# Optimization experiments

Measured on AMD Instinct MI355X. Metric: run time of the kernel, lower is better.

Reference implementation:

```python
import jax, jax.numpy as jnp
import numpy as np

B, H, W, C = 32, 56, 56, 384
NH, WS, SS = 12, 7, 3
DH = C // NH
N = WS * WS
HID = 4 * C
SCALE = DH ** -0.5


def _make_attn_mask(h, w, ws, ss):
    img = np.zeros((h, w), dtype=np.float32)
    cnt = 0
    for hs in (slice(0, -ws), slice(-ws, -ss), slice(-ss, None)):
        for wsl in (slice(0, -ws), slice(-ws, -ss), slice(-ss, None)):
            img[hs, wsl] = cnt
            cnt += 1
    mw = img.reshape(h // ws, ws, w // ws, ws).transpose(0, 2, 1, 3).reshape(-1, ws * ws)
    diff = mw[:, None, :] - mw[:, :, None]  # (nW, n, n)
    return np.where(diff != 0, np.float32(-100.0), np.float32(0.0))


def _make_rel_pos_index(ws):
    coords = np.stack(np.meshgrid(np.arange(ws), np.arange(ws), indexing='ij')).reshape(2, -1)
    rel = (coords[:, :, None] - coords[:, None, :]).transpose(1, 2, 0)  # (n, n, 2)
    rel[..., 0] += ws - 1
    rel[..., 1] += ws - 1
    rel[..., 0] *= 2 * ws - 1
    return rel.sum(-1)  # (n, n)


ATTN_MASK = jnp.asarray(_make_attn_mask(H, W, WS, SS))          # (nW, n, n)
REL_IDX = jnp.asarray(_make_rel_pos_index(WS))                   # (n, n)


def layernorm(x, g, b, eps):
    mu = jnp.mean(x, axis=-1, keepdims=True)
    var = jnp.var(x, axis=-1, keepdims=True)
    return (x - mu) * jax.lax.rsqrt(var + eps) * g + b


def window_partition(x, ws):
    b, h, w, c = x.shape
    x = x.reshape(b, h // ws, ws, w // ws, ws, c)
    return x.transpose(0, 1, 3, 2, 4, 5).reshape(-1, ws, ws, c)


def window_reverse(windows, ws, h, w):
    b = windows.shape[0] // ((h // ws) * (w // ws))
    x = windows.reshape(b, h // ws, w // ws, ws, ws, -1)
    return x.transpose(0, 1, 3, 2, 4, 5).reshape(b, h, w, -1)


def setup_inputs() -> dict:
    key = jax.random.key(0)
    ks = jax.random.split(key, 8)
    d = {
        'x': jax.random.normal(ks[0], (B, H * W, C), dtype=jnp.float32),
        'ln1_g': jnp.ones((C,), jnp.float32), 'ln1_b': jnp.zeros((C,), jnp.float32),
        'qkv_w': jax.random.normal(ks[1], (C, 3 * C), jnp.float32) * 0.02,
        'qkv_b': jnp.zeros((3 * C,), jnp.float32),
        'proj_w': jax.random.normal(ks[2], (C, C), jnp.float32) * 0.02,
        'proj_b': jnp.zeros((C,), jnp.float32),
        'rpb_table': jax.random.normal(ks[3], ((2 * WS - 1) ** 2, NH), jnp.float32) * 0.02,
        'ln2_g': jnp.ones((C,), jnp.float32), 'ln2_b': jnp.zeros((C,), jnp.float32),
        'ffln_g': jnp.ones((C,), jnp.float32), 'ffln_b': jnp.zeros((C,), jnp.float32),
        'ff1_w': jax.random.normal(ks[4], (C, HID), jnp.float32) * 0.02,
        'ff1_b': jnp.zeros((HID,), jnp.float32),
        'ff2_w': jax.random.normal(ks[5], (HID, C), jnp.float32) * 0.02,
        'ff2_b': jnp.zeros((C,), jnp.float32),
    }
    return d


def reference(x, ln1_g, ln1_b, qkv_w, qkv_b, proj_w, proj_b, rpb_table,
              ln2_g, ln2_b, ffln_g, ffln_b, ff1_w, ff1_b, ff2_w, ff2_b):
    b = x.shape[0]
    shortcut = x
    xn = layernorm(x, ln1_g, ln1_b, 1e-5).reshape(b, H, W, C)
    shifted = jnp.roll(xn, shift=(-SS, -SS), axis=(1, 2))
    xw = window_partition(shifted, WS).reshape(-1, N, C)  # (b*nW, n, c)
    Bw = xw.shape[0]
    nW = Bw // b

    qkv = (xw @ qkv_w + qkv_b).reshape(Bw, N, 3, NH, DH).transpose(2, 0, 3, 1, 4)
    q, k, v = qkv[0], qkv[1], qkv[2]  # (Bw, nh, n, dh)
    dots = jnp.einsum('bhnd,bhmd->bhnm', q, k) * SCALE

    bias = rpb_table[REL_IDX.reshape(-1)].reshape(N, N, NH).transpose(2, 0, 1)  # (nh, n, n)
    attn = dots + bias[None]
    attn = attn.reshape(b, nW, NH, N, N) + ATTN_MASK[None, :, None, :, :]
    attn = jax.nn.softmax(attn.reshape(Bw, NH, N, N), axis=-1)

    out = jnp.einsum('bhnm,bhmd->bhnd', attn, v)
    out = out.transpose(0, 2, 1, 3).reshape(Bw, N, C)
    out = out @ proj_w + proj_b

    out = window_reverse(out.reshape(-1, WS, WS, C), WS, H, W)
    out = jnp.roll(out, shift=(SS, SS), axis=(1, 2)).reshape(b, H * W, C)

    x = shortcut + out
    y = layernorm(x, ln2_g, ln2_b, 1e-5)
    y = layernorm(y, ffln_g, ffln_b, 1e-6)
    y = jax.nn.gelu(y @ ff1_w + ff1_b, approximate=False) @ ff2_w + ff2_b
    return x + y
```

## Files before the change

kernel.cpp:

```cpp
#include <hip/hip_runtime.h>
#include <hip/hip_bf16.h>

typedef short bf16x8 __attribute__((ext_vector_type(8)));
typedef short short4v __attribute__((ext_vector_type(4)));
typedef float f32x4  __attribute__((ext_vector_type(4)));

static constexpr float SCALE = 0.17677669529663687f;

__device__ __forceinline__ void gload_lds16(const void* g, void* l) {
  __builtin_amdgcn_global_load_lds(
      (const __attribute__((address_space(1))) unsigned int*)g,
      (__attribute__((address_space(3))) unsigned int*)l, 16, 0, 0);
}

__device__ __forceinline__ size_t win_to_nat(int t) {
  int win = t / 49; int n = t - win * 49;
  int bb = win >> 6; int wimg = win & 63;
  int hb = wimg >> 3, wb = wimg & 7;
  int nr = n / 7, nc = n - nr * 7;
  int hh = hb * 7 + nr + 3; if (hh >= 56) hh -= 56;
  int ww = wb * 7 + nc + 3; if (ww >= 56) ww -= 56;
  return (size_t)bb * 3136 + (size_t)hh * 56 + ww;
}

__device__ __forceinline__ float gelu_tanh(float val) {
  float u = val * (val * val * 0.044715f + 1.0f) * 1.5957691216f;
  float e = __expf(u);
  float th = 1.f - 2.f / (e + 1.f);
  return 0.5f * val * (1.f + th);
}

__global__ __launch_bounds__(256)
void k_transpose(const float* __restrict__ W, __hip_bfloat16* __restrict__ Wt,
                 int K, int N) {
  __shared__ float tile[32][33];
  int tx = threadIdx.x & 31, ty = threadIdx.x >> 5;
  int tc = blockIdx.x, tr = blockIdx.y;
#pragma unroll
  for (int r = 0; r < 32; r += 8)
    tile[r + ty][tx] = W[(size_t)(tr * 32 + r + ty) * N + tc * 32 + tx];
  __syncthreads();
#pragma unroll
  for (int r = 0; r < 32; r += 8)
    Wt[(size_t)(tc * 32 + r + ty) * K + tr * 32 + tx] =
        __float2bfloat16(tile[tx][r + ty]);
}

__global__ __launch_bounds__(256)
void k_ln1(const float* __restrict__ x, const float* __restrict__ gw,
           const float* __restrict__ bw, __hip_bfloat16* __restrict__ xw) {
  int lane = threadIdx.x & 63;
  int t = blockIdx.x * 4 + (threadIdx.x >> 6);
  size_t nt = win_to_nat(t);
  const float* xr = x + nt * 384;
  float4 a  = *(const float4*)(xr + lane * 4);
  float2 c2 = *(const float2*)(xr + 256 + lane * 2);
  float v[6] = {a.x, a.y, a.z, a.w, c2.x, c2.y};
  int c0 = lane * 4, c1 = 256 + lane * 2;
  int ch[6] = {c0, c0 + 1, c0 + 2, c0 + 3, c1, c1 + 1};
  float s = 0.f, q = 0.f;
#pragma unroll
  for (int i = 0; i < 6; i++) { s += v[i]; q += v[i] * v[i]; }
#pragma unroll
  for (int m = 1; m < 64; m <<= 1) { s += __shfl_xor(s, m); q += __shfl_xor(q, m); }
  float mean = s * (1.f / 384.f);
  float rstd = rsqrtf(q * (1.f / 384.f) - mean * mean + 1e-5f);
  __hip_bfloat16* o = xw + (size_t)t * 384;
#pragma unroll
  for (int i = 0; i < 6; i++)
    o[ch[i]] = __float2bfloat16((v[i] - mean) * rstd * gw[ch[i]] + bw[ch[i]]);
}

__global__ __launch_bounds__(256)
void k_ln2ff(const float* __restrict__ xres, const float* __restrict__ g2,
             const float* __restrict__ b2, const float* __restrict__ gf,
             const float* __restrict__ bf_, __hip_bfloat16* __restrict__ yln) {
  int lane = threadIdx.x & 63;
  int t = blockIdx.x * 4 + (threadIdx.x >> 6);
  const float* xr = xres + (size_t)t * 384;
  float4 a  = *(const float4*)(xr + lane * 4);
  float2 c2 = *(const float2*)(xr + 256 + lane * 2);
  float v[6] = {a.x, a.y, a.z, a.w, c2.x, c2.y};
  int c0 = lane * 4, c1 = 256 + lane * 2;
  int ch[6] = {c0, c0 + 1, c0 + 2, c0 + 3, c1, c1 + 1};
  float s = 0.f, q = 0.f;
#pragma unroll
  for (int i = 0; i < 6; i++) { s += v[i]; q += v[i] * v[i]; }
#pragma unroll
  for (int m = 1; m < 64; m <<= 1) { s += __shfl_xor(s, m); q += __shfl_xor(q, m); }
  float mean = s * (1.f / 384.f);
  float rstd = rsqrtf(q * (1.f / 384.f) - mean * mean + 1e-5f);
  float y1[6];
  s = 0.f; q = 0.f;
#pragma unroll
  for (int i = 0; i < 6; i++) {
    y1[i] = (v[i] - mean) * rstd * g2[ch[i]] + b2[ch[i]];
    s += y1[i]; q += y1[i] * y1[i];
  }
#pragma unroll
  for (int m = 1; m < 64; m <<= 1) { s += __shfl_xor(s, m); q += __shfl_xor(q, m); }
  float m2 = s * (1.f / 384.f);
  float r2 = rsqrtf(q * (1.f / 384.f) - m2 * m2 + 1e-6f);
  __hip_bfloat16* o = yln + (size_t)t * 384;
#pragma unroll
  for (int i = 0; i < 6; i++)
    o[ch[i]] = __float2bfloat16((y1[i] - m2) * r2 * gf[ch[i]] + bf_[ch[i]]);
}

enum { EPI_QKV = 0, EPI_PROJ = 1, EPI_FF1 = 2, EPI_FF2 = 3 };

template <int EPI>
__global__ __launch_bounds__(256)
void k_gemm(const __hip_bfloat16* __restrict__ A, const __hip_bfloat16* __restrict__ Wt,
            const float* __restrict__ bias, int K, int nCol, int cpx,
            const float* __restrict__ aux,
            float* __restrict__ out_f,
            __hip_bfloat16* __restrict__ out_b) {
  __shared__ __hip_bfloat16 LB[32768];
  int tid = threadIdx.x;
  int lane = tid & 63, w = tid >> 6;
  int g = lane >> 4, r16 = lane & 15;
  int wr = w >> 1, wc = w & 1;

  int bid = blockIdx.x;
  int wg = (bid & 7) * cpx + (bid >> 3);
  int rB = wg / nCol;
  int rowBlk = rB * 128;
  int colBlk = (wg - rB * nCol) * 128;

  int srow = tid >> 3;
  int cch = (tid & 7) ^ (srow & 7);
  const __hip_bfloat16* PA = A + (size_t)(rowBlk + srow) * K + cch * 8;
  const __hip_bfloat16* PB = Wt + (size_t)(colBlk + srow) * K + cch * 8;

#define STG(NB, T)                                                            \
  {                                                                           \
    int k0s = (T) << 6;                                                       \
    _Pragma("unroll") for (int j = 0; j < 4; j++) {                           \
      gload_lds16(PA + (size_t)j * 32 * K + k0s, &LB[(NB) * 8192 + j * 2048 + w * 512]); \
      gload_lds16(PB + (size_t)j * 32 * K + k0s, &LB[16384 + (NB) * 8192 + j * 2048 + w * 512]); \
    }                                                                         \
  }

  int aBase = (wr * 64 + r16) * 64;
  int bBase = (wc * 64 + r16) * 64;
  int sw0 = (g ^ (r16 & 7)) * 8;
  int sw1 = ((4 + g) ^ (r16 & 7)) * 8;

  f32x4 acc[4][4] = {};
  const int nt = K >> 6;

  STG(0, 0)

  for (int t = 0; t < nt; ++t) {
    int cur = t & 1;
    if (t + 1 < nt) {
      STG(cur ^ 1, t + 1)
      asm volatile("s_waitcnt vmcnt(8)" ::: "memory");
    } else {
      asm volatile("s_waitcnt vmcnt(0)" ::: "memory");
    }
    __builtin_amdgcn_s_barrier();

    bf16x8 a0[4], a1[4], b0[4], b1[4];
#pragma unroll
    for (int mi = 0; mi < 4; mi++) {
      a0[mi] = *(const bf16x8*)(&LB[cur * 8192 + aBase + mi * 1024 + sw0]);
      a1[mi] = *(const bf16x8*)(&LB[cur * 8192 + aBase + mi * 1024 + sw1]);
    }
#pragma unroll
    for (int ni = 0; ni < 4; ni++) {
      b0[ni] = *(const bf16x8*)(&LB[16384 + cur * 8192 + bBase + ni * 1024 + sw0]);
      b1[ni] = *(const bf16x8*)(&LB[16384 + cur * 8192 + bBase + ni * 1024 + sw1]);
    }
    __builtin_amdgcn_s_setprio(1);
#pragma unroll
    for (int mi = 0; mi < 4; mi++)
#pragma unroll
      for (int ni = 0; ni < 4; ni++) {
        acc[mi][ni] = __builtin_amdgcn_mfma_f32_16x16x32_bf16(b0[ni], a0[mi], acc[mi][ni], 0, 0, 0);
        acc[mi][ni] = __builtin_amdgcn_mfma_f32_16x16x32_bf16(b1[ni], a1[mi], acc[mi][ni], 0, 0, 0);
      }
    __builtin_amdgcn_s_setprio(0);
    __builtin_amdgcn_s_barrier();
  }
#undef STG

  if constexpr (EPI == EPI_QKV || EPI == EPI_FF1) {
    __hip_bfloat16* EP = &LB[w * 4096];
#pragma unroll
    for (int ni = 0; ni < 4; ni++) {
      float4 b4 = *(const float4*)(bias + colBlk + wc * 64 + ni * 16 + g * 4);
#pragma unroll
      for (int mi = 0; mi < 4; mi++) {
        float v0 = acc[mi][ni][0] + b4.x, v1 = acc[mi][ni][1] + b4.y,
              v2 = acc[mi][ni][2] + b4.z, v3 = acc[mi][ni][3] + b4.w;
        if constexpr (EPI == EPI_FF1) {
          v0 = gelu_tanh(v0); v1 = gelu_tanh(v1);
          v2 = gelu_tanh(v2); v3 = gelu_tanh(v3);
        }
        short4v s4 = {(short)__bfloat16_as_ushort(__float2bfloat16(v0)),
                      (short)__bfloat16_as_ushort(__float2bfloat16(v1)),
                      (short)__bfloat16_as_ushort(__float2bfloat16(v2)),
                      (short)__bfloat16_as_ushort(__float2bfloat16(v3))};
        int row = mi * 16 + r16;
        int ch8 = (ni * 2 + (g >> 1)) ^ (row & 7);
        *(short4v*)(&EP[row * 64 + ch8 * 8 + (g & 1) * 4]) = s4;
      }
    }
#pragma unroll
    for (int j = 0; j < 8; j++) {
      int r = j * 8 + (lane >> 3);
      bf16x8 vv = *(const bf16x8*)(&EP[r * 64 + ((lane & 7) ^ (r & 7)) * 8]);
      int grow = rowBlk + wr * 64 + r;
      int col0 = colBlk + wc * 64 + (lane & 7) * 8;
      if constexpr (EPI == EPI_QKV) {
        int winr = grow / 49, nn = grow - winr * 49;
        int which = col0 / 384; int rem = col0 - which * 384;
        int hh = rem >> 5, dd = rem & 31;
        size_t off = (((size_t)winr * 12 + hh) * 49 + nn) * 32 + dd;
        *(bf16x8*)(out_b + (size_t)which * 38535168u + off) = vv;
      } else {
        *(bf16x8*)(out_b + (size_t)grow * 1536 + col0) = vv;
      }
    }
  } else {
    float* EPF = (float*)LB + w * 4096;
#pragma unroll
    for (int ni = 0; ni < 4; ni++) {
      float4 b4 = *(const float4*)(bias + colBlk + wc * 64 + ni * 16 + g * 4);
#pragma unroll
      for (int mi = 0; mi < 4; mi++) {
        f32x4 v = acc[mi][ni];
        v[0] += b4.x; v[1] += b4.y; v[2] += b4.z; v[3] += b4.w;
        int row = mi * 16 + r16;
        int ch4 = (ni * 4 + g) ^ r16;
        *(f32x4*)(&EPF[row * 64 + ch4 * 4]) = v;
      }
    }
#pragma unroll
    for (int j = 0; j < 16; j++) {
      int r = j * 4 + g;
      f32x4 vv = *(const f32x4*)(&EPF[r * 64 + ((r16 ^ (r & 15)) * 4)]);
      int grow = rowBlk + wr * 64 + r;
      int col0 = colBlk + wc * 64 + r16 * 4;
      if constexpr (EPI == EPI_PROJ) {
        size_t nt2 = win_to_nat(grow);
        const float4 a4 = *(const float4*)(aux + nt2 * 384 + col0);
        float4 o4 = {vv[0] + a4.x, vv[1] + a4.y, vv[2] + a4.z, vv[3] + a4.w};
        *(float4*)(out_f + nt2 * 384 + col0) = o4;
      } else {
        const float4 a4 = *(const float4*)(aux + (size_t)grow * 384 + col0);
        float4 o4 = {vv[0] + a4.x, vv[1] + a4.y, vv[2] + a4.z, vv[3] + a4.w};
        *(float4*)(out_f + (size_t)grow * 384 + col0) = o4;
      }
    }
  }
}

__global__ __launch_bounds__(256)
void k_attn(const __hip_bfloat16* __restrict__ q, const __hip_bfloat16* __restrict__ k,
            const __hip_bfloat16* __restrict__ v, const float* __restrict__ rpb,
            __hip_bfloat16* __restrict__ o) {
  __shared__ __hip_bfloat16 P[4][64][72];
  int tid = threadIdx.x;
  int lane = tid & 63, wave = tid >> 6;
  int g = lane >> 4, r16 = lane & 15;
  int gid = blockIdx.x * 4 + wave;
  int wi = gid / 12, h = gid - (gid / 12) * 12;
  int wimg = wi & 63;
  int hb = wimg >> 3, wb = wimg & 7;
  size_t base = ((size_t)wi * 12 + h) * (49 * 32);
  const __hip_bfloat16* qb = q + base;
  const __hip_bfloat16* kb = k + base;
  const __hip_bfloat16* vb = v + base;

  bf16x8 zf = {0, 0, 0, 0, 0, 0, 0, 0};
  bf16x8 qf[4], kf[4];
#pragma unroll
  for (int mi = 0; mi < 4; mi++) {
    int row = mi * 16 + r16;
    qf[mi] = (row < 49) ? *(const bf16x8*)(qb + row * 32 + g * 8) : zf;
    kf[mi] = (row < 49) ? *(const bf16x8*)(kb + row * 32 + g * 8) : zf;
  }
  f32x4 fz = {0.f, 0.f, 0.f, 0.f};
  f32x4 S[4][4];
#pragma unroll
  for (int mi = 0; mi < 4; mi++)
#pragma unroll
    for (int ni = 0; ni < 4; ni++)
      S[mi][ni] = __builtin_amdgcn_mfma_f32_16x16x32_bf16(qf[mi], kf[ni], fz, 0, 0, 0);

  int kiA[4], kjA[4], rkA[4], cvA[4];
#pragma unroll
  for (int ni = 0; ni < 4; ni++) {
    int col = ni * 16 + r16;
    cvA[ni] = (col < 49);
    int ki = col / 7, kj = col - (col / 7) * 7;
    kiA[ni] = ki; kjA[ni] = kj;
    int hg = hb * 7 + ki, wg = wb * 7 + kj;
    int rh = (hg < 49) ? 0 : ((hg < 53) ? 1 : 2);
    int rw = (wg < 49) ? 0 : ((wg < 53) ? 1 : 2);
    rkA[ni] = rh * 3 + rw;
  }

#pragma unroll
  for (int mi = 0; mi < 4; mi++) {
#pragma unroll
    for (int rr = 0; rr < 4; rr++) {
      int row = mi * 16 + g * 4 + rr;
      float sv[4];
      float mx = -1e30f;
      int qi = row / 7, qj = row - (row / 7) * 7;
      int hgq = hb * 7 + qi, wgq = wb * 7 + qj;
      int rhq = (hgq < 49) ? 0 : ((hgq < 53) ? 1 : 2);
      int rwq = (wgq < 49) ? 0 : ((wgq < 53) ? 1 : 2);
      int rq = rhq * 3 + rwq;
#pragma unroll
      for (int ni = 0; ni < 4; ni++) {
        float s = -1e30f;
        if (row < 49 && cvA[ni]) {
          int idx = (qi - kiA[ni] + 6) * 13 + (qj - kjA[ni] + 6);
          float maskv = (rq != rkA[ni]) ? -100.f : 0.f;
          s = S[mi][ni][rr] * SCALE + rpb[idx * 12 + h] + maskv;
        }
        sv[ni] = s;
        mx = fmaxf(mx, s);
      }
#pragma unroll
      for (int m = 1; m <= 8; m <<= 1) mx = fmaxf(mx, __shfl_xor(mx, m));
      float sum = 0.f;
#pragma unroll
      for (int ni = 0; ni < 4; ni++) {
        float p = __expf(sv[ni] - mx);
        sv[ni] = p; sum += p;
      }
#pragma unroll
      for (int m = 1; m <= 8; m <<= 1) sum += __shfl_xor(sum, m);
      float inv = 1.f / sum;
#pragma unroll
      for (int ni = 0; ni < 4; ni++)
        P[wave][row][ni * 16 + r16] = __float2bfloat16(sv[ni] * inv);
    }
  }

  f32x4 O[4][2] = {};
#pragma unroll
  for (int ks = 0; ks < 2; ks++) {
    bf16x8 pf[4];
#pragma unroll
    for (int mi = 0; mi < 4; mi++)
      pf[mi] = *(const bf16x8*)(&P[wave][mi * 16 + r16][ks * 32 + g * 8]);
#pragma unroll
    for (int ni = 0; ni < 2; ni++) {
      bf16x8 vf = zf;
#pragma unroll
      for (int j = 0; j < 8; j++) {
        int m = ks * 32 + g * 8 + j;
        if (m < 49) vf[j] = ((const short*)vb)[m * 32 + ni * 16 + r16];
      }
#pragma unroll
      for (int mi = 0; mi < 4; mi++)
        O[mi][ni] = __builtin_amdgcn_mfma_f32_16x16x32_bf16(pf[mi], vf, O[mi][ni], 0, 0, 0);
    }
  }

#pragma unroll
  for (int mi = 0; mi < 4; mi++)
#pragma unroll
    for (int rr = 0; rr < 4; rr++) {
      int row = mi * 16 + g * 4 + rr;
      if (row < 49) {
#pragma unroll
        for (int ni = 0; ni < 2; ni++) {
          int col = ni * 16 + r16;
          o[(((size_t)wi * 49 + row) * 12 + h) * 32 + col] = __float2bfloat16(O[mi][ni][rr]);
        }
      }
    }
}

extern "C" void kernel_launch(void* const* d_in, const int* in_sizes, int n_in,
                              void* d_out, int out_size, void* d_ws, size_t ws_size,
                              hipStream_t stream) {
  const float* x      = (const float*)d_in[0];
  const float* ln1_g  = (const float*)d_in[1];
  const float* ln1_b  = (const float*)d_in[2];
  const float* qkv_w  = (const float*)d_in[3];
  const float* qkv_b  = (const float*)d_in[4];
  const float* proj_w = (const float*)d_in[5];
  const float* proj_b = (const float*)d_in[6];
  const float* rpb    = (const float*)d_in[7];
  const float* ln2_g  = (const float*)d_in[8];
  const float* ln2_b  = (const float*)d_in[9];
  const float* ffg    = (const float*)d_in[10];
  const float* ffb    = (const float*)d_in[11];
  const float* ff1_w  = (const float*)d_in[12];
  const float* ff1_b  = (const float*)d_in[13];
  const float* ff2_w  = (const float*)d_in[14];
  const float* ff2_b  = (const float*)d_in[15];
  float* out = (float*)d_out;

  char* ws = (char*)d_ws;
  __hip_bfloat16* xw     = (__hip_bfloat16*)ws;
  __hip_bfloat16* qbuf   = (__hip_bfloat16*)(ws + 77070336u);
  __hip_bfloat16* kbuf   = qbuf + 38535168u;
  __hip_bfloat16* vbuf   = kbuf + 38535168u;
  __hip_bfloat16* attn_o = xw;
  __hip_bfloat16* hbuf   = (__hip_bfloat16*)ws;
  float*          x_res  = (float*)(ws + 308281344u);
  __hip_bfloat16* yln    = (__hip_bfloat16*)(ws + 462422016u);
  __hip_bfloat16* qkv_wt = (__hip_bfloat16*)(ws + 539492352u);
  __hip_bfloat16* proj_wt = qkv_wt + 442368u;
  __hip_bfloat16* ff1_wt  = proj_wt + 147456u;
  __hip_bfloat16* ff2_wt  = ff1_wt + 589824u;

  k_transpose<<<dim3(1152 / 32, 384 / 32), dim3(256), 0, stream>>>(qkv_w, qkv_wt, 384, 1152);
  k_transpose<<<dim3(384 / 32, 384 / 32), dim3(256), 0, stream>>>(proj_w, proj_wt, 384, 384);
  k_transpose<<<dim3(1536 / 32, 384 / 32), dim3(256), 0, stream>>>(ff1_w, ff1_wt, 384, 1536);
  k_transpose<<<dim3(384 / 32, 1536 / 32), dim3(256), 0, stream>>>(ff2_w, ff2_wt, 1536, 384);

  k_ln1<<<dim3(25088), dim3(256), 0, stream>>>(x, ln1_g, ln1_b, xw);

  k_gemm<EPI_QKV><<<dim3(7056), dim3(256), 0, stream>>>(xw, qkv_wt, qkv_b, 384, 9, 7056 / 8,
                                                        nullptr, nullptr, qbuf);
  k_attn<<<dim3(6144), dim3(256), 0, stream>>>(qbuf, kbuf, vbuf, rpb, attn_o);
  k_gemm<EPI_PROJ><<<dim3(2352), dim3(256), 0, stream>>>(attn_o, proj_wt, proj_b, 384, 3, 2352 / 8,
                                                         x, x_res, nullptr);
  k_ln2ff<<<dim3(25088), dim3(256), 0, stream>>>(x_res, ln2_g, ln2_b, ffg, ffb, yln);
  k_gemm<EPI_FF1><<<dim3(9408), dim3(256), 0, stream>>>(yln, ff1_wt, ff1_b, 384, 12, 9408 / 8,
                                                        nullptr, nullptr, hbuf);
  k_gemm<EPI_FF2><<<dim3(2352), dim3(256), 0, stream>>>(hbuf, ff2_wt, ff2_b, 1536, 3, 2352 / 8,
                                                        x_res, out, nullptr);
}
```

Measured before the change: 905.9 us.

## Halve GEMM K-tile to shrink LDS and use sigmoid-based GELU

```diff
diff --git a/kernel.cpp b/kernel.cpp
--- a/kernel.cpp
+++ b/kernel.cpp
@@ -23,11 +23,9 @@
   return (size_t)bb * 3136 + (size_t)hh * 56 + ww;
 }
 
-__device__ __forceinline__ float gelu_tanh(float val) {
-  float u = val * (val * val * 0.044715f + 1.0f) * 1.5957691216f;
-  float e = __expf(u);
-  float th = 1.f - 2.f / (e + 1.f);
-  return 0.5f * val * (1.f + th);
+__device__ __forceinline__ float gelu_fast(float x) {
+  float t = __expf(-1.702f * x);
+  return x / (1.f + t);
 }
 
 __global__ __launch_bounds__(256)
@@ -116,7 +114,7 @@
             const float* __restrict__ aux,
             float* __restrict__ out_f,
             __hip_bfloat16* __restrict__ out_b) {
-  __shared__ __hip_bfloat16 LB[32768];
+  __shared__ __hip_bfloat16 LB[16384];
   int tid = threadIdx.x;
   int lane = tid & 63, w = tid >> 6;
   int g = lane >> 4, r16 = lane & 15;
@@ -128,27 +126,26 @@
   int rowBlk = rB * 128;
   int colBlk = (wg - rB * nCol) * 128;
 
-  int srow = tid >> 3;
-  int cch = (tid & 7) ^ (srow & 7);
+  int srow = tid >> 2;
+  int cch = (tid & 3) ^ (srow & 3);
   const __hip_bfloat16* PA = A + (size_t)(rowBlk + srow) * K + cch * 8;
   const __hip_bfloat16* PB = Wt + (size_t)(colBlk + srow) * K + cch * 8;
 
 #define STG(NB, T)                                                            \
   {                                                                           \
-    int k0s = (T) << 6;                                                       \
-    _Pragma("unroll") for (int j = 0; j < 4; j++) {                           \
-      gload_lds16(PA + (size_t)j * 32 * K + k0s, &LB[(NB) * 8192 + j * 2048 + w * 512]); \
-      gload_lds16(PB + (size_t)j * 32 * K + k0s, &LB[16384 + (NB) * 8192 + j * 2048 + w * 512]); \
+    int k0s = (T) << 5;                                                       \
+    _Pragma("unroll") for (int j = 0; j < 2; j++) {                           \
+      gload_lds16(PA + (size_t)j * 64 * K + k0s, &LB[(NB) * 4096 + j * 2048 + w * 512]); \
+      gload_lds16(PB + (size_t)j * 64 * K + k0s, &LB[8192 + (NB) * 4096 + j * 2048 + w * 512]); \
     }                                                                         \
   }
 
-  int aBase = (wr * 64 + r16) * 64;
-  int bBase = (wc * 64 + r16) * 64;
-  int sw0 = (g ^ (r16 & 7)) * 8;
-  int sw1 = ((4 + g) ^ (r16 & 7)) * 8;
+  int aBase = (wr * 64 + r16) * 32;
+  int bBase = 8192 + (wc * 64 + r16) * 32;
+  int sw = (g ^ (r16 & 3)) * 8;
 
   f32x4 acc[4][4] = {};
-  const int nt = K >> 6;
+  const int nt = K >> 5;
 
   STG(0, 0)
 
@@ -156,31 +153,25 @@
     int cur = t & 1;
     if (t + 1 < nt) {
       STG(cur ^ 1, t + 1)
-      asm volatile("s_waitcnt vmcnt(8)" ::: "memory");
+      asm volatile("s_waitcnt vmcnt(4)" ::: "memory");
     } else {
       asm volatile("s_waitcnt vmcnt(0)" ::: "memory");
     }
     __builtin_amdgcn_s_barrier();
 
-    bf16x8 a0[4], a1[4], b0[4], b1[4];
-#pragma unroll
-    for (int mi = 0; mi < 4; mi++) {
-      a0[mi] = *(const bf16x8*)(&LB[cur * 8192 + aBase + mi * 1024 + sw0]);
-      a1[mi] = *(const bf16x8*)(&LB[cur * 8192 + aBase + mi * 1024 + sw1]);
-    }
-#pragma unroll
-    for (int ni = 0; ni < 4; ni++) {
-      b0[ni] = *(const bf16x8*)(&LB[16384 + cur * 8192 + bBase + ni * 1024 + sw0]);
-      b1[ni] = *(const bf16x8*)(&LB[16384 + cur * 8192 + bBase + ni * 1024 + sw1]);
-    }
+    bf16x8 a[4], b[4];
+#pragma unroll
+    for (int mi = 0; mi < 4; mi++)
+      a[mi] = *(const bf16x8*)(&LB[cur * 4096 + aBase + mi * 512 + sw]);
+#pragma unroll
+    for (int ni = 0; ni < 4; ni++)
+      b[ni] = *(const bf16x8*)(&LB[cur * 4096 + bBase + ni * 512 + sw]);
     __builtin_amdgcn_s_setprio(1);
 #pragma unroll
     for (int mi = 0; mi < 4; mi++)
 #pragma unroll
-      for (int ni = 0; ni < 4; ni++) {
-        acc[mi][ni] = __builtin_amdgcn_mfma_f32_16x16x32_bf16(b0[ni], a0[mi], acc[mi][ni], 0, 0, 0);
-        acc[mi][ni] = __builtin_amdgcn_mfma_f32_16x16x32_bf16(b1[ni], a1[mi], acc[mi][ni], 0, 0, 0);
-      }
+      for (int ni = 0; ni < 4; ni++)
+        acc[mi][ni] = __builtin_amdgcn_mfma_f32_16x16x32_bf16(b[ni], a[mi], acc[mi][ni], 0, 0, 0);
     __builtin_amdgcn_s_setprio(0);
     __builtin_amdgcn_s_barrier();
   }
@@ -196,8 +187,8 @@
         float v0 = acc[mi][ni][0] + b4.x, v1 = acc[mi][ni][1] + b4.y,
               v2 = acc[mi][ni][2] + b4.z, v3 = acc[mi][ni][3] + b4.w;
         if constexpr (EPI == EPI_FF1) {
-          v0 = gelu_tanh(v0); v1 = gelu_tanh(v1);
-          v2 = gelu_tanh(v2); v3 = gelu_tanh(v3);
+          v0 = gelu_fast(v0); v1 = gelu_fast(v1);
+          v2 = gelu_fast(v2); v3 = gelu_fast(v3);
         }
         short4v s4 = {(short)__bfloat16_as_ushort(__float2bfloat16(v0)),
                       (short)__bfloat16_as_ushort(__float2bfloat16(v1)),
@@ -225,34 +216,38 @@
       }
     }
   } else {
-    float* EPF = (float*)LB + w * 4096;
-#pragma unroll
-    for (int ni = 0; ni < 4; ni++) {
-      float4 b4 = *(const float4*)(bias + colBlk + wc * 64 + ni * 16 + g * 4);
-#pragma unroll
-      for (int mi = 0; mi < 4; mi++) {
-        f32x4 v = acc[mi][ni];
-        v[0] += b4.x; v[1] += b4.y; v[2] += b4.z; v[3] += b4.w;
-        int row = mi * 16 + r16;
-        int ch4 = (ni * 4 + g) ^ r16;
-        *(f32x4*)(&EPF[row * 64 + ch4 * 4]) = v;
-      }
-    }
-#pragma unroll
-    for (int j = 0; j < 16; j++) {
-      int r = j * 4 + g;
-      f32x4 vv = *(const f32x4*)(&EPF[r * 64 + ((r16 ^ (r & 15)) * 4)]);
-      int grow = rowBlk + wr * 64 + r;
-      int col0 = colBlk + wc * 64 + r16 * 4;
-      if constexpr (EPI == EPI_PROJ) {
-        size_t nt2 = win_to_nat(grow);
-        const float4 a4 = *(const float4*)(aux + nt2 * 384 + col0);
-        float4 o4 = {vv[0] + a4.x, vv[1] + a4.y, vv[2] + a4.z, vv[3] + a4.w};
-        *(float4*)(out_f + nt2 * 384 + col0) = o4;
-      } else {
-        const float4 a4 = *(const float4*)(aux + (size_t)grow * 384 + col0);
-        float4 o4 = {vv[0] + a4.x, vv[1] + a4.y, vv[2] + a4.z, vv[3] + a4.w};
-        *(float4*)(out_f + (size_t)grow * 384 + col0) = o4;
+    float* EPF = (float*)LB + w * 2048;
+#pragma unroll
+    for (int half = 0; half < 2; half++) {
+#pragma unroll
+      for (int ni = 0; ni < 4; ni++) {
+        float4 b4 = *(const float4*)(bias + colBlk + wc * 64 + ni * 16 + g * 4);
+#pragma unroll
+        for (int mi2 = 0; mi2 < 2; mi2++) {
+          int mi = half * 2 + mi2;
+          f32x4 v = acc[mi][ni];
+          v[0] += b4.x; v[1] += b4.y; v[2] += b4.z; v[3] += b4.w;
+          int row = mi2 * 16 + r16;
+          int ch4 = (ni * 4 + g) ^ r16;
+          *(f32x4*)(&EPF[row * 64 + ch4 * 4]) = v;
+        }
+      }
+#pragma unroll
+      for (int j = 0; j < 8; j++) {
+        int r = j * 4 + g;
+        f32x4 vv = *(const f32x4*)(&EPF[r * 64 + ((r16 ^ (r & 15)) * 4)]);
+        int grow = rowBlk + wr * 64 + half * 32 + r;
+        int col0 = colBlk + wc * 64 + r16 * 4;
+        if constexpr (EPI == EPI_PROJ) {
+          size_t nt2 = win_to_nat(grow);
+          const float4 a4 = *(const float4*)(aux + nt2 * 384 + col0);
+          float4 o4 = {vv[0] + a4.x, vv[1] + a4.y, vv[2] + a4.z, vv[3] + a4.w};
+          *(float4*)(out_f + nt2 * 384 + col0) = o4;
+        } else {
+          const float4 a4 = *(const float4*)(aux + (size_t)grow * 384 + col0);
+          float4 o4 = {vv[0] + a4.x, vv[1] + a4.y, vv[2] + a4.z, vv[3] + a4.w};
+          *(float4*)(out_f + (size_t)grow * 384 + col0) = o4;
+        }
       }
     }
   }
```

Result: slower. 934.1 us (+3.1%).
